# Kernel optimization log

Hardware: AMD Instinct MI355X
Metric: run time of the kernel (lower is better)

Reference implementation:

```python
import jax, jax.numpy as jnp
import numpy as np

N = 4_194_304   # samples per polarization
L = 513         # impulse response taps


def setup_inputs() -> dict:
    key = jax.random.key(0)
    k1, k2, k3, k4 = jax.random.split(key, 4)
    tx_real = jax.random.normal(k1, (2, N), dtype=jnp.float32)
    tx_imag = jax.random.normal(k2, (2, N), dtype=jnp.float32)
    h_real = jax.random.normal(k3, (L,), dtype=jnp.float32)
    h_imag = jax.random.normal(k4, (L,), dtype=jnp.float32)
    return {"tx_real": tx_real, "tx_imag": tx_imag, "h_real": h_real, "h_imag": h_imag}


def reference(tx_real, tx_imag, h_real, h_imag):
    # Dual-pol complex baseband signal [2, N]; same taps h [L] applied to each pol.
    tx = tx_real + 1j * tx_imag          # complex64 [2, N]
    h = h_real + 1j * h_imag             # complex64 [L]
    n_out = tx.shape[-1] + h.shape[0] - 1  # 'full' convolution length
    # FFT-based full convolution, both polarizations batched in one FFT call
    # (mathematically identical to overlap-save convolution in 'full' mode).
    X = jnp.fft.fft(tx, n=n_out, axis=-1)   # [2, n_out]
    H = jnp.fft.fft(h, n=n_out)             # [n_out]
    y = jnp.fft.ifft(X * H[None, :], axis=-1)  # [2, n_out] complex
    # Return real/imag stacked so the output is a real array: [2, n_out, 2]
    return jnp.stack([y.real, y.imag], axis=-1)
```

## Files before the change

kernel.cpp:

```cpp
#include <hip/hip_runtime.h>
#include <hip/hip_bf16.h>


#define NSAMP 4194304
#define LTAPS 513
#define NOUT  (NSAMP + LTAPS - 1)

#define BLK       256
#define WAVE_OUT  1024
#define BLOCK_OUT 2048
#define HALO      512
#define XELEMS    (BLOCK_OUT + HALO + 16)
#define NB        34
#define HROWS     568
#define NBLK      ((NOUT + BLOCK_OUT - 1) / BLOCK_OUT)

typedef __attribute__((ext_vector_type(8)))  short short8;
typedef __attribute__((ext_vector_type(4)))  short short4v;
typedef __attribute__((ext_vector_type(4)))  int   int4v;
typedef __attribute__((ext_vector_type(16))) float float16v;

__device__ __forceinline__ int xswz(int e) { return e + ((e >> 5) << 3); }
#define XSZ 3224

__device__ __forceinline__ short f2b(float f) {
    __bf16 b = (__bf16)f;
    return __builtin_bit_cast(short, b);
}

__global__ __launch_bounds__(BLK)
void build_h(const float* __restrict__ hr, const float* __restrict__ hi,
             short* __restrict__ hh) {
    int R = blockIdx.x * BLK + threadIdx.x;
    if (R < HROWS) {
        short8 vr, vi;
        #pragma unroll
        for (int j = 0; j < 8; ++j) {
            int idx = R - 24 - j;
            bool ok = (idx >= 0) && (idx < LTAPS);
            vr[j] = f2b(ok ? hr[idx] : 0.0f);
            vi[j] = f2b(ok ? hi[idx] : 0.0f);
        }
        *(short8*)(hh + (size_t)(0 * HROWS + R) * 8) = vr;
        *(short8*)(hh + (size_t)(1 * HROWS + R) * 8) = vi;
    }
}

#define MFMA32(A, B, C) __builtin_amdgcn_mfma_f32_32x32x16_bf16((A), (B), (C), 0, 0, 0)

__device__ __forceinline__ short8 bneg8(short8 v) {
    int4v t = __builtin_bit_cast(int4v, v);
    t ^= (int4v){(int)0x80008000, (int)0x80008000, (int)0x80008000, (int)0x80008000};
    return __builtin_bit_cast(short8, t);
}

__global__ __launch_bounds__(BLK, 5)
void fir_mfma32w(const float* __restrict__ txr_all, const float* __restrict__ txi_all,
                 const short* __restrict__ hh, float2* __restrict__ out) {
    const int N0  = blockIdx.x * BLOCK_OUT;
    const int tid = threadIdx.x;

    __shared__ __align__(16) short xr_s[2][XSZ];
    __shared__ __align__(16) short xi_s[2][XSZ];

    #pragma unroll
    for (int p = 0; p < 2; ++p) {
        const float* __restrict__ xr_g = txr_all + (size_t)p * NSAMP;
        const float* __restrict__ xi_g = txi_all + (size_t)p * NSAMP;
        #pragma unroll
        for (int it = 0; it < 3; ++it) {
            int e = (tid + it * BLK) * 4;
            if (e < XELEMS) {
                int g = N0 - HALO + e;
                float r0, r1, r2, r3, i0, i1, i2, i3;
                if (g >= 0 && g + 3 < NSAMP) {
                    float4 fr = *(const float4*)(xr_g + g);
                    float4 fi = *(const float4*)(xi_g + g);
                    r0 = fr.x; r1 = fr.y; r2 = fr.z; r3 = fr.w;
                    i0 = fi.x; i1 = fi.y; i2 = fi.z; i3 = fi.w;
                } else {
                    int gc0 = min(max(g + 0, 0), NSAMP - 1);
                    int gc1 = min(max(g + 1, 0), NSAMP - 1);
                    int gc2 = min(max(g + 2, 0), NSAMP - 1);
                    int gc3 = min(max(g + 3, 0), NSAMP - 1);
                    r0 = (g + 0 >= 0 && g + 0 < NSAMP) ? xr_g[gc0] : 0.0f;
                    r1 = (g + 1 >= 0 && g + 1 < NSAMP) ? xr_g[gc1] : 0.0f;
                    r2 = (g + 2 >= 0 && g + 2 < NSAMP) ? xr_g[gc2] : 0.0f;
                    r3 = (g + 3 >= 0 && g + 3 < NSAMP) ? xr_g[gc3] : 0.0f;
                    i0 = (g + 0 >= 0 && g + 0 < NSAMP) ? xi_g[gc0] : 0.0f;
                    i1 = (g + 1 >= 0 && g + 1 < NSAMP) ? xi_g[gc1] : 0.0f;
                    i2 = (g + 2 >= 0 && g + 2 < NSAMP) ? xi_g[gc2] : 0.0f;
                    i3 = (g + 3 >= 0 && g + 3 < NSAMP) ? xi_g[gc3] : 0.0f;
                }
                int ls = xswz(e);
                short4v vr = { f2b(r0), f2b(r1), f2b(r2), f2b(r3) };
                short4v vi = { f2b(i0), f2b(i1), f2b(i2), f2b(i3) };
                *(short4v*)(&xr_s[p][ls]) = vr;
                *(short4v*)(&xi_s[p][ls]) = vi;
            }
        }
    }
    __syncthreads();

    const int lane = tid & 63;
    const int wave = tid >> 6;
    const int pol  = wave >> 1;
    const int strip = wave & 1;
    const int cc   = lane & 31;
    const int half = lane >> 5;

    float16v acc_re = {0.f,0.f,0.f,0.f,0.f,0.f,0.f,0.f,0.f,0.f,0.f,0.f,0.f,0.f,0.f,0.f};
    float16v acc_im = acc_re;

    const int    ebase = HALO + strip * WAVE_OUT + 32 * cc + 8 * half + 16;
    const short* hp0   = hh + (size_t)(cc - 8 * half + 8) * 8;
    const short* xrp   = xr_s[pol];
    const short* xip   = xi_s[pol];

    for (int b = 0; b < NB; ++b) {
        const short* hp = hp0 + (size_t)(16 * b) * 8;
        short8 fhr = *(const short8*)(hp);
        short8 fhi = *(const short8*)(hp + (size_t)HROWS * 8);
        int ls = xswz(ebase - 16 * b);
        short8 fxr = *(const short8*)(xrp + ls);
        short8 fxi = *(const short8*)(xip + ls);
        short8 fnxi = bneg8(fxi);
        acc_re = MFMA32(fxr,  fhr, acc_re);
        acc_re = MFMA32(fnxi, fhi, acc_re);
        acc_im = MFMA32(fxi,  fhr, acc_im);
        acc_im = MFMA32(fxr,  fhi, acc_im);
    }

    float2* __restrict__ op = out + (size_t)pol * NOUT;
    const int nw = N0 + strip * WAVE_OUT;
    #pragma unroll
    for (int v = 0; v < 16; ++v) {
        int row = (v & 3) + 8 * (v >> 2) + 4 * half;
        int n = nw + 32 * row + cc;
        if (n < NOUT) op[n] = make_float2(acc_re[v], acc_im[v]);
    }
}

extern "C" void kernel_launch(void* const* d_in, const int* in_sizes, int n_in,
                              void* d_out, int out_size, void* d_ws, size_t ws_size,
                              hipStream_t stream) {
    const float* txr = (const float*)d_in[0];
    const float* txi = (const float*)d_in[1];
    const float* hr  = (const float*)d_in[2];
    const float* hi  = (const float*)d_in[3];
    float2* out = (float2*)d_out;
    short* hh = (short*)d_ws;

    build_h<<<dim3((HROWS + BLK - 1) / BLK), BLK, 0, stream>>>(hr, hi, hh);

    fir_mfma32w<<<dim3(NBLK), BLK, 0, stream>>>(txr, txi, hh, out);
}
```

Baseline: 142.9 us.

## Process both polarizations per wave, sharing tap fragments across four accumulators

```diff
diff --git a/kernel.cpp b/kernel.cpp
--- a/kernel.cpp
+++ b/kernel.cpp
@@ -8,7 +8,7 @@
 
 #define BLK       256
 #define WAVE_OUT  1024
-#define BLOCK_OUT 2048
+#define BLOCK_OUT 4096
 #define HALO      512
 #define XELEMS    (BLOCK_OUT + HALO + 16)
 #define NB        34
@@ -21,7 +21,7 @@
 typedef __attribute__((ext_vector_type(16))) float float16v;
 
 __device__ __forceinline__ int xswz(int e) { return e + ((e >> 5) << 3); }
-#define XSZ 3224
+#define XSZ 5776
 
 __device__ __forceinline__ short f2b(float f) {
     __bf16 b = (__bf16)f;
@@ -54,7 +54,7 @@
     return __builtin_bit_cast(short8, t);
 }
 
-__global__ __launch_bounds__(BLK, 5)
+__global__ __launch_bounds__(BLK, 3)
 void fir_mfma32w(const float* __restrict__ txr_all, const float* __restrict__ txi_all,
                  const short* __restrict__ hh, float2* __restrict__ out) {
     const int N0  = blockIdx.x * BLOCK_OUT;
@@ -68,7 +68,7 @@
         const float* __restrict__ xr_g = txr_all + (size_t)p * NSAMP;
         const float* __restrict__ xi_g = txi_all + (size_t)p * NSAMP;
         #pragma unroll
-        for (int it = 0; it < 3; ++it) {
+        for (int it = 0; it < 5; ++it) {
             int e = (tid + it * BLK) * 4;
             if (e < XELEMS) {
                 int g = N0 - HALO + e;
@@ -102,42 +102,54 @@
     }
     __syncthreads();
 
-    const int lane = tid & 63;
-    const int wave = tid >> 6;
-    const int pol  = wave >> 1;
-    const int strip = wave & 1;
-    const int cc   = lane & 31;
-    const int half = lane >> 5;
+    const int lane  = tid & 63;
+    const int wave  = tid >> 6;
+    const int strip = wave;
+    const int cc    = lane & 31;
+    const int half  = lane >> 5;
 
-    float16v acc_re = {0.f,0.f,0.f,0.f,0.f,0.f,0.f,0.f,0.f,0.f,0.f,0.f,0.f,0.f,0.f,0.f};
-    float16v acc_im = acc_re;
+    float16v zero = {0.f,0.f,0.f,0.f,0.f,0.f,0.f,0.f,0.f,0.f,0.f,0.f,0.f,0.f,0.f,0.f};
+    float16v acc_re0 = zero, acc_im0 = zero, acc_re1 = zero, acc_im1 = zero;
 
     const int    ebase = HALO + strip * WAVE_OUT + 32 * cc + 8 * half + 16;
     const short* hp0   = hh + (size_t)(cc - 8 * half + 8) * 8;
-    const short* xrp   = xr_s[pol];
-    const short* xip   = xi_s[pol];
+    const short* xr0p  = xr_s[0];
+    const short* xi0p  = xi_s[0];
+    const short* xr1p  = xr_s[1];
+    const short* xi1p  = xi_s[1];
 
     for (int b = 0; b < NB; ++b) {
         const short* hp = hp0 + (size_t)(16 * b) * 8;
         short8 fhr = *(const short8*)(hp);
         short8 fhi = *(const short8*)(hp + (size_t)HROWS * 8);
         int ls = xswz(ebase - 16 * b);
-        short8 fxr = *(const short8*)(xrp + ls);
-        short8 fxi = *(const short8*)(xip + ls);
-        short8 fnxi = bneg8(fxi);
-        acc_re = MFMA32(fxr,  fhr, acc_re);
-        acc_re = MFMA32(fnxi, fhi, acc_re);
-        acc_im = MFMA32(fxi,  fhr, acc_im);
-        acc_im = MFMA32(fxr,  fhi, acc_im);
+        short8 fxr0 = *(const short8*)(xr0p + ls);
+        short8 fxi0 = *(const short8*)(xi0p + ls);
+        short8 fxr1 = *(const short8*)(xr1p + ls);
+        short8 fxi1 = *(const short8*)(xi1p + ls);
+        short8 fnxi0 = bneg8(fxi0);
+        short8 fnxi1 = bneg8(fxi1);
+        acc_re0 = MFMA32(fxr0,  fhr, acc_re0);
+        acc_im0 = MFMA32(fxi0,  fhr, acc_im0);
+        acc_re1 = MFMA32(fxr1,  fhr, acc_re1);
+        acc_im1 = MFMA32(fxi1,  fhr, acc_im1);
+        acc_re0 = MFMA32(fnxi0, fhi, acc_re0);
+        acc_im0 = MFMA32(fxr0,  fhi, acc_im0);
+        acc_re1 = MFMA32(fnxi1, fhi, acc_re1);
+        acc_im1 = MFMA32(fxr1,  fhi, acc_im1);
     }
 
-    float2* __restrict__ op = out + (size_t)pol * NOUT;
+    float2* __restrict__ op0 = out;
+    float2* __restrict__ op1 = out + (size_t)NOUT;
     const int nw = N0 + strip * WAVE_OUT;
     #pragma unroll
     for (int v = 0; v < 16; ++v) {
         int row = (v & 3) + 8 * (v >> 2) + 4 * half;
         int n = nw + 32 * row + cc;
-        if (n < NOUT) op[n] = make_float2(acc_re[v], acc_im[v]);
+        if (n < NOUT) {
+            op0[n] = make_float2(acc_re0[v], acc_im0[v]);
+            op1[n] = make_float2(acc_re1[v], acc_im1[v]);
+        }
     }
 }
 
```

Result: no change. 142.3 us (-0.4%).
